# Optimization experiments

Measured on AMD Instinct MI355X. Metric: run time of the kernel, lower is better.

The kernel has to match this reference:

```python
import jax, jax.numpy as jnp
import numpy as np

PRECISION_RATIO = 0.1
ROUTE_THRESH = 0.05

def ternary_quantize(W):
    # TWN-style: delta = 0.7*mean|W|, alpha = mean of kept magnitudes
    delta = 0.7 * jnp.mean(jnp.abs(W))
    mask = (jnp.abs(W) > delta).astype(W.dtype)
    alpha = jnp.sum(jnp.abs(W) * mask) / jnp.maximum(jnp.sum(mask), 1.0)
    return alpha * jnp.sign(W) * mask

def rpb_weight(W, precision_ratio=PRECISION_RATIO):
    # Ternary base + full-precision residual kept for top `precision_ratio` of entries
    Wq = ternary_quantize(W)
    res = W - Wq
    k = max(1, int(precision_ratio * W.size))
    kth = jax.lax.top_k(jnp.abs(res).reshape(-1), k)[0][-1]
    keep = (jnp.abs(res) >= kth).astype(W.dtype)
    return Wq + res * keep

def selective_route(x, threshold=ROUTE_THRESH):
    return x * (jnp.abs(x) >= threshold).astype(x.dtype)

def _lin(x, W, b):
    return x @ W.T + b

def setup_inputs() -> dict:
    key = jax.random.key(0)
    ks = jax.random.split(key, 24)
    B = 8192
    dims = {"vision": 2048, "text": 1024, "audio": 512}
    D = 1024
    T = D * 3  # total_dim = 3072
    s = 0.02
    inp = {
        "x_vision": jax.random.normal(ks[0], (B, dims["vision"]), jnp.float32),
        "x_text": jax.random.normal(ks[1], (B, dims["text"]), jnp.float32),
        "x_audio": jax.random.normal(ks[2], (B, dims["audio"]), jnp.float32),
        "Wv": jax.random.normal(ks[3], (D, dims["vision"]), jnp.float32) * s,
        "bv": jnp.zeros((D,), jnp.float32),
        "Wt": jax.random.normal(ks[4], (D, dims["text"]), jnp.float32) * s,
        "bt": jnp.zeros((D,), jnp.float32),
        "Wa": jax.random.normal(ks[5], (D, dims["audio"]), jnp.float32) * s,
        "ba": jnp.zeros((D,), jnp.float32),
        "Wq1": jax.random.normal(ks[6], (D, T), jnp.float32) * s,
        "bq1": jnp.zeros((D,), jnp.float32),
        "Wq2": jax.random.normal(ks[7], (D, D), jnp.float32) * s,
        "bq2": jnp.zeros((D,), jnp.float32),
        "Wf1": jax.random.normal(ks[8], (D, T), jnp.float32) * s,
        "bf1": jnp.zeros((D,), jnp.float32),
        "Wf2": jax.random.normal(ks[9], (D, D), jnp.float32) * s,
        "bf2": jnp.zeros((D,), jnp.float32),
        "mix_ratio": jnp.asarray(0.75, jnp.float32),
    }
    return inp

def reference(x_vision, x_text, x_audio, Wv, bv, Wt, bt, Wa, ba,
              Wq1, bq1, Wq2, bq2, Wf1, bf1, Wf2, bf2, mix_ratio):
    # per-modality projections then concat in modality order
    pv = _lin(x_vision, Wv, bv)
    pt = _lin(x_text, Wt, bt)
    pa = _lin(x_audio, Wa, ba)
    concat = jnp.concatenate([pv, pt, pa], axis=1)  # [B, 3*D]
    routed = selective_route(concat)
    # quantized (RPB) branch
    h = jax.nn.relu(_lin(routed, rpb_weight(Wq1), bq1))
    out_quant = _lin(h, rpb_weight(Wq2), bq2)
    # full-precision branch
    g = jax.nn.relu(_lin(concat, Wf1, bf1))
    out_full = _lin(g, Wf2, bf2)
    mix = jax.nn.sigmoid(mix_ratio)
    return mix * out_quant + (1.0 - mix) * out_full
```

## Files before the change

### kernel.cpp

```cpp
#include <hip/hip_runtime.h>


typedef _Float16 f16x8 __attribute__((ext_vector_type(8)));
typedef float f32x4 __attribute__((ext_vector_type(4)));

__device__ __forceinline__ unsigned short f16b(float v) {
  union { _Float16 h; unsigned short u; } cv; cv.h = (_Float16)v; return cv.u;
}

__device__ __forceinline__ void load_lds16(const void* g, void* l) {
  __builtin_amdgcn_global_load_lds(
      (const __attribute__((address_space(1))) void*)g,
      (__attribute__((address_space(3))) void*)l, 16, 0, 0);
}

__device__ __forceinline__ float sigmoidf_dev(float x) {
  return 1.0f / (1.0f + expf(-x));
}

#define NB_W1 768
#define NB_TOT 1024

__device__ __forceinline__ float reduce_region_f(const float* part, int lo, int hi,
                                                 float* sbuf) {
  float a = 0.f;
  for (int i = lo + threadIdx.x; i < hi; i += 256) a += part[i];
  sbuf[threadIdx.x] = a; __syncthreads();
  for (int o = 128; o > 0; o >>= 1) {
    if ((int)threadIdx.x < o) sbuf[threadIdx.x] += sbuf[threadIdx.x + o];
    __syncthreads();
  }
  float r = sbuf[0];
  __syncthreads();
  return r;
}

__device__ __forceinline__ float alpha_region(const float* pb, const unsigned* pc,
                                              int lo, int hi, float* sf, unsigned* sc) {
  float a = 0.f; unsigned c = 0;
  for (int i = lo + threadIdx.x; i < hi; i += 256) { a += pb[i]; c += pc[i]; }
  sf[threadIdx.x] = a; sc[threadIdx.x] = c; __syncthreads();
  for (int o = 128; o > 0; o >>= 1) {
    if ((int)threadIdx.x < o) { sf[threadIdx.x] += sf[threadIdx.x + o]; sc[threadIdx.x] += sc[threadIdx.x + o]; }
    __syncthreads();
  }
  float s = sf[0]; float cnt = (float)sc[0];
  __syncthreads();
  if (cnt < 1.f) cnt = 1.f;
  return s / cnt;
}

__device__ __forceinline__ unsigned radix_prefix(const unsigned* __restrict__ hists,
                                                 int w, int nr, unsigned k,
                                                 unsigned* sscan, unsigned* res2) {
  int t = threadIdx.x;
  unsigned prefix = 0, krem = k;
  for (int rr = 0; rr < nr; ++rr) {
    sscan[t] = hists[(rr * 2 + w) * 256 + (255 - t)];
    __syncthreads();
#pragma unroll
    for (int o = 1; o < 256; o <<= 1) {
      unsigned add = (t >= o) ? sscan[t - o] : 0u;
      __syncthreads();
      sscan[t] += add;
      __syncthreads();
    }
    if (sscan[t] >= krem && (t == 0 || sscan[t - 1] < krem)) {
      res2[0] = (unsigned)(255 - t);
      res2[1] = (t == 0) ? 0u : sscan[t - 1];
    }
    __syncthreads();
    prefix |= res2[0] << (24 - 8 * rr);
    krem -= res2[1];
    __syncthreads();
  }
  return prefix;
}

struct Pre1Args {
  const float* src[7];
  unsigned short* dst[7];
  long cum4[8];
  const float* W1; long n41;
  const float* W2; long n42;
  float* part;
  unsigned* hists;
};

__global__ void pre1(Pre1Args a) {
  if (blockIdx.x < 2048) {
    long total = a.cum4[7];
    for (long i = (long)blockIdx.x * 256 + threadIdx.x; i < total;
         i += (long)2048 * 256) {
      int s = 0;
#pragma unroll
      for (int j = 1; j < 7; ++j) s += (i >= a.cum4[j]) ? 1 : 0;
      long off = i - a.cum4[s];
      float4 v = ((const float4*)a.src[s])[off];
      ushort4 o;
      o.x = f16b(v.x); o.y = f16b(v.y); o.z = f16b(v.z); o.w = f16b(v.w);
      ((ushort4*)a.dst[s])[off] = o;
    }
  } else {
    __shared__ float s[256];
    int bid2 = (int)blockIdx.x - 2048;
    if (bid2 < 8) a.hists[bid2 * 256 + threadIdx.x] = 0;
    int w = bid2 < NB_W1 ? 0 : 1;
    const float4* W4 = (const float4*)(w ? a.W2 : a.W1);
    long n4 = w ? a.n42 : a.n41;
    int nb = w ? (NB_TOT - NB_W1) : NB_W1;
    int bid = w ? bid2 - NB_W1 : bid2;
    float acc = 0.f;
    for (long i = (long)bid * 256 + threadIdx.x; i < n4;
         i += (long)nb * 256) {
      float4 v = W4[i];
      acc += fabsf(v.x) + fabsf(v.y) + fabsf(v.z) + fabsf(v.w);
    }
    s[threadIdx.x] = acc; __syncthreads();
    for (int o = 128; o > 0; o >>= 1) {
      if ((int)threadIdx.x < o) s[threadIdx.x] += s[threadIdx.x + o];
      __syncthreads();
    }
    if (threadIdx.x == 0) a.part[bid2] = s[0];
  }
}

__global__ void hist_r(const float* __restrict__ W1, long S1v,
                       const float* __restrict__ W2, long S2v,
                       const float* __restrict__ part,
                       const float* __restrict__ pb, const unsigned* __restrict__ pc,
                       unsigned* __restrict__ hists, int round,
                       unsigned k1, unsigned k2) {
  __shared__ float sf[256]; __shared__ unsigned sc[256];
  __shared__ unsigned h[256]; __shared__ unsigned sscan[256];
  __shared__ unsigned res2[2];
  int t = threadIdx.x;
  int w = blockIdx.x < NB_W1 ? 0 : 1;
  const float* W = w ? W2 : W1;
  long S = w ? S2v : S1v;
  int nb = w ? (NB_TOT - NB_W1) : NB_W1;
  int bid = w ? (int)blockIdx.x - NB_W1 : (int)blockIdx.x;
  int lo = w ? NB_W1 : 0, hi = w ? NB_TOT : NB_W1;
  float tot = reduce_region_f(part, lo, hi, sf);
  float delta = 0.7f * (tot / (float)S);
  float alpha = alpha_region(pb, pc, lo, hi, sf, sc);
  unsigned prefix = radix_prefix(hists, w, round, w ? k2 : k1, sscan, res2);
  h[t] = 0;
  __syncthreads();
  int shift = 24 - 8 * round;
  int hs = shift + 8;
  for (long i = (long)bid * 256 + t; i < S; i += (long)nb * 256) {
    float x = W[i];
    float aw = fabsf(x);
    float wq = (aw > delta) ? copysignf(alpha, x) : 0.0f;
    unsigned ub = __float_as_uint(fabsf(x - wq));
    bool ok = (hs >= 32) || ((ub >> hs) == (prefix >> hs));
    if (ok) atomicAdd(&h[(ub >> shift) & 255u], 1u);
  }
  __syncthreads();
  if (h[t]) atomicAdd(&hists[(round * 2 + w) * 256 + t], h[t]);
}

struct FinArgs {
  const float* Wq1; const float* Wq2; const float* Wf2;
  const float* bq2; const float* bf2; const float* mixp;
  const float* part; const float* pb; const unsigned* pc;
  const unsigned* hists;
  unsigned k1, k2;
  unsigned short* wq1_h;
  unsigned short* w2_h;
  float* b2;
};

__global__ void finalize_weights(FinArgs a) {
  __shared__ float sf[256]; __shared__ unsigned sc[256];
  __shared__ unsigned sscan[256]; __shared__ unsigned res2[2];
  const long S1 = 3145728, S2 = 1048576, D = 1024;
  float tot1 = reduce_region_f(a.part, 0, NB_W1, sf);
  float d1 = 0.7f * (tot1 / (float)S1);
  float tot2 = reduce_region_f(a.part, NB_W1, NB_TOT, sf);
  float d2 = 0.7f * (tot2 / (float)S2);
  float a1 = alpha_region(a.pb, a.pc, 0, NB_W1, sf, sc);
  float a2 = alpha_region(a.pb, a.pc, NB_W1, NB_TOT, sf, sc);
  unsigned kth1 = radix_prefix(a.hists, 0, 4, a.k1, sscan, res2);
  unsigned kth2 = radix_prefix(a.hists, 1, 4, a.k2, sscan, res2);
  float mix = sigmoidf_dev(a.mixp[0]);
  long total = S1 + 2 * S2 + D;
  for (long i = (long)blockIdx.x * blockDim.x + threadIdx.x; i < total;
       i += (long)gridDim.x * blockDim.x) {
    if (i < S1) {
      float x = a.Wq1[i];
      float wq = (fabsf(x) > d1) ? copysignf(a1, x) : 0.0f;
      float res = x - wq;
      float v = wq + ((__float_as_uint(fabsf(res)) >= kth1) ? res : 0.0f);
      a.wq1_h[i] = f16b(v);
    } else if (i < S1 + S2) {
      long j = i - S1; int r = (int)(j >> 10), c = (int)(j & 1023);
      float x = a.Wq2[j];
      float wq = (fabsf(x) > d2) ? copysignf(a2, x) : 0.0f;
      float res = x - wq;
      float v = wq + ((__float_as_uint(fabsf(res)) >= kth2) ? res : 0.0f);
      a.w2_h[(long)r * 2048 + c] = f16b(mix * v);
    } else if (i < S1 + 2 * S2) {
      long j = i - S1 - S2; int r = (int)(j >> 10), c = (int)(j & 1023);
      a.w2_h[(long)r * 2048 + 1024 + c] = f16b((1.0f - mix) * a.Wf2[j]);
    } else {
      long j = i - S1 - 2 * S2;
      a.b2[j] = mix * a.bq2[j] + (1.0f - mix) * a.bf2[j];
    }
  }
}

struct GemmArgs {
  const unsigned short* A0; const unsigned short* A1; const unsigned short* A2;
  const unsigned short* B0; const unsigned short* B1; const unsigned short* B2;
  const float* c0; const float* c1; const float* c2;
  int K0, K1, K2;
  int nrows;
  int ldc;
  int cpsl;
  int nwg;
  unsigned short* o0; unsigned short* o1; float* oF;
  const float* pkW1; long pkS1;
  const float* pkW2; long pkS2;
  const float* pkPart; float* pkPb; unsigned* pkPc;
};

template <int EPI, int BN, bool PK>
__global__ __launch_bounds__(512) void gemm9(GemmArgs g) {
  constexpr int AL = 128 * 32 * 2;
  constexpr int BL = BN * 32 * 2;
  constexpr int BISS = BL / 8192;
  constexpr int NR = BN / 4 / 16;
  __shared__ __align__(16) char sm[2 * AL + 2 * BL];
  const int tid = threadIdx.x;

  if constexpr (PK) {
    if ((int)blockIdx.x >= g.nwg) {
      float* sf = (float*)sm;
      unsigned* sc = (unsigned*)(sm + 2048);
      int bid2 = (int)blockIdx.x - g.nwg;
      int w = bid2 < NB_W1 ? 0 : 1;
      const float* W = w ? g.pkW2 : g.pkW1;
      long S = w ? g.pkS2 : g.pkS1;
      int nb = w ? (NB_TOT - NB_W1) : NB_W1;
      int bid = w ? bid2 - NB_W1 : bid2;
      if (tid < 256) {
        float a = 0.f;
        for (int i = (w ? NB_W1 : 0) + tid; i < (w ? NB_TOT : NB_W1); i += 256)
          a += g.pkPart[i];
        sf[tid] = a;
      }
      __syncthreads();
      for (int o = 128; o > 0; o >>= 1) {
        if (tid < o) sf[tid] += sf[tid + o];
        __syncthreads();
      }
      float delta = 0.7f * (sf[0] / (float)S);
      __syncthreads();
      float a = 0.f; unsigned c = 0;
      for (long i = (long)bid * 512 + tid; i < S; i += (long)nb * 512) {
        float aw = fabsf(W[i]);
        if (aw > delta) { a += aw; ++c; }
      }
      sf[tid] = a; sc[tid] = c; __syncthreads();
      for (int o = 256; o > 0; o >>= 1) {
        if (tid < o) { sf[tid] += sf[tid + o]; sc[tid] += sc[tid + o]; }
        __syncthreads();
      }
      if (tid == 0) { g.pkPb[bid2] = sf[0]; g.pkPc[bid2] = sc[0]; }
      return;
    }
  }

  const int wid = tid >> 6;
  const int lane = tid & 63;
  const int wm = wid >> 2, wn = wid & 3;

  const int nwg = g.nwg;
  const int id = (blockIdx.x & 7) * (nwg >> 3) + (blockIdx.x >> 3);
  const int ncols = nwg / g.nrows;
  const int c = id % ncols, r = id / ncols;
  const int sel = c >> g.cpsl, lc = c & ((1 << g.cpsl) - 1);

  const unsigned short* A = sel == 0 ? g.A0 : (sel == 1 ? g.A1 : g.A2);
  const unsigned short* Bw = sel == 0 ? g.B0 : (sel == 1 ? g.B1 : g.B2);
  const float* bias = sel == 0 ? g.c0 : (sel == 1 ? g.c1 : g.c2);
  const int K = sel == 0 ? g.K0 : (sel == 1 ? g.K1 : g.K2);
  const long brow = (long)r * 128;
  const int bRowB = lc * BN;

  f32x4 acc[4][NR];
#pragma unroll
  for (int i = 0; i < 4; ++i)
#pragma unroll
    for (int j = 0; j < NR; ++j)
#pragma unroll
      for (int e = 0; e < 4; ++e) acc[i][j][e] = 0.f;

  const int oA = tid * 16;
  const unsigned short* aSrc = A + (brow + (oA >> 6)) * (long)K + ((oA & 63) >> 1);
  const unsigned short* bSrc[BISS];
#pragma unroll
  for (int j = 0; j < BISS; ++j) {
    int o = j * 8192 + tid * 16;
    bSrc[j] = Bw + (long)(bRowB + (o >> 6)) * K + ((o & 63) >> 1);
  }

  auto STAGE = [&](int buf, int k0) {
    load_lds16(aSrc + k0, sm + (size_t)buf * AL + wid * 1024);
#pragma unroll
    for (int j = 0; j < BISS; ++j)
      load_lds16(bSrc[j] + k0, sm + 2 * AL + (size_t)buf * BL + j * 8192 + wid * 1024);
  };

  const int kb = (lane >> 4) * 16;
  auto COMPUTE = [&](int buf) {
    const char* lAp = sm + (size_t)buf * AL;
    const char* lBp = sm + 2 * AL + (size_t)buf * BL;
    f16x8 a[4], b[NR];
#pragma unroll
    for (int m = 0; m < 4; ++m)
      a[m] = *(const f16x8*)(lAp + (wm * 64 + m * 16 + (lane & 15)) * 64 + kb);
#pragma unroll
    for (int n = 0; n < NR; ++n)
      b[n] = *(const f16x8*)(lBp + (wn * (BN / 4) + n * 16 + (lane & 15)) * 64 + kb);
#pragma unroll
    for (int m = 0; m < 4; ++m)
#pragma unroll
      for (int n = 0; n < NR; ++n)
        acc[m][n] = __builtin_amdgcn_mfma_f32_16x16x32_f16(a[m], b[n], acc[m][n], 0, 0, 0);
  };

  const int NT = K >> 5;
  STAGE(0, 0);
  __syncthreads();
  int cur = 0;
  for (int t = 0; t < NT - 1; ++t) {
    STAGE(cur ^ 1, (t + 1) << 5);
    COMPUTE(cur);
    __syncthreads();
    cur ^= 1;
  }
  COMPUTE(cur);

  const int cb = c * BN + wn * (BN / 4);
  const int rb = r * 128 + wm * 64;
  const int bcol0 = bRowB + wn * (BN / 4);
#pragma unroll
  for (int i = 0; i < 4; ++i) {
    int r0 = rb + i * 16 + ((lane >> 4) << 2);
#pragma unroll
    for (int j = 0; j < NR; ++j) {
      int ccol = cb + j * 16 + (lane & 15);
      float bb = bias[bcol0 + j * 16 + (lane & 15)];
#pragma unroll
      for (int e = 0; e < 4; ++e) {
        float v = acc[i][j][e] + bb;
        long idx = (long)(r0 + e) * g.ldc + ccol;
        if constexpr (EPI == 0) {
          g.o0[idx] = f16b(v);
          g.o1[idx] = f16b(fabsf(v) >= 0.05f ? v : 0.0f);
        } else if constexpr (EPI == 1) {
          g.o0[idx] = f16b(fmaxf(v, 0.0f));
        } else {
          g.oF[idx] = v;
        }
      }
    }
  }
}

extern "C" void kernel_launch(void* const* d_in, const int* in_sizes, int n_in,
                              void* d_out, int out_size, void* d_ws, size_t ws_size,
                              hipStream_t stream) {
  const float* xv = (const float*)d_in[0];
  const float* xt = (const float*)d_in[1];
  const float* xa = (const float*)d_in[2];
  const float* Wv = (const float*)d_in[3];
  const float* bv = (const float*)d_in[4];
  const float* Wt = (const float*)d_in[5];
  const float* bt = (const float*)d_in[6];
  const float* Wa = (const float*)d_in[7];
  const float* ba = (const float*)d_in[8];
  const float* Wq1 = (const float*)d_in[9];
  const float* bq1 = (const float*)d_in[10];
  const float* Wq2 = (const float*)d_in[11];
  const float* bq2 = (const float*)d_in[12];
  const float* Wf1 = (const float*)d_in[13];
  const float* bf1 = (const float*)d_in[14];
  const float* Wf2 = (const float*)d_in[15];
  const float* bf2 = (const float*)d_in[16];
  const float* mixp = (const float*)d_in[17];

  const int B = 8192, D = 1024, T = 3072;
  const int Kv = 2048, Kt = 1024, Ka = 512;
  const long S1 = (long)D * T, S2 = (long)D * D;

  char* w = (char*)d_ws;
  auto alloc = [&](size_t bytes) -> char* {
    char* p = w; w += (bytes + 255) & ~(size_t)255; return p;
  };
  unsigned short* xv_h = (unsigned short*)alloc((size_t)B * Kv * 2);
  unsigned short* xt_h = (unsigned short*)alloc((size_t)B * Kt * 2);
  unsigned short* xa_h = (unsigned short*)alloc((size_t)B * Ka * 2);
  unsigned short* wv_h = (unsigned short*)alloc((size_t)D * Kv * 2);
  unsigned short* wt_h = (unsigned short*)alloc((size_t)D * Kt * 2);
  unsigned short* wa_h = (unsigned short*)alloc((size_t)D * Ka * 2);
  unsigned short* wq1_h = (unsigned short*)alloc((size_t)D * T * 2);
  unsigned short* wf1_h = (unsigned short*)alloc((size_t)D * T * 2);
  unsigned short* w2_h = (unsigned short*)alloc((size_t)D * 2048 * 2);
  unsigned short* concat_h = (unsigned short*)alloc((size_t)B * T * 2);
  unsigned short* routed_h = (unsigned short*)alloc((size_t)B * T * 2);
  unsigned short* a2_h = (unsigned short*)alloc((size_t)B * 2048 * 2);
  float* b2 = (float*)alloc(D * 4);
  float* part = (float*)alloc(1024 * 4);
  float* pb = (float*)alloc(1024 * 4);
  unsigned* pc = (unsigned*)alloc(1024 * 4);
  unsigned* hists = (unsigned*)alloc(4 * 2 * 256 * 4);

  const unsigned k1 = (unsigned)(S1 / 10), k2 = (unsigned)(S2 / 10);

  Pre1Args pa;
  pa.src[0] = xv;  pa.dst[0] = xv_h;
  pa.src[1] = xt;  pa.dst[1] = xt_h;
  pa.src[2] = xa;  pa.dst[2] = xa_h;
  pa.src[3] = Wv;  pa.dst[3] = wv_h;
  pa.src[4] = Wt;  pa.dst[4] = wt_h;
  pa.src[5] = Wa;  pa.dst[5] = wa_h;
  pa.src[6] = Wf1; pa.dst[6] = wf1_h;
  long n4s[7] = {(long)B * Kv / 4, (long)B * Kt / 4, (long)B * Ka / 4,
                 (long)D * Kv / 4, (long)D * Kt / 4, (long)D * Ka / 4, S1 / 4};
  pa.cum4[0] = 0;
  for (int i = 0; i < 7; ++i) pa.cum4[i + 1] = pa.cum4[i] + n4s[i];
  pa.W1 = Wq1; pa.n41 = S1 / 4;
  pa.W2 = Wq2; pa.n42 = S2 / 4;
  pa.part = part; pa.hists = hists;
  pre1<<<3072, 256, 0, stream>>>(pa);

  GemmArgs gp;
  gp.A0 = xv_h; gp.A1 = xt_h; gp.A2 = xa_h;
  gp.B0 = wv_h; gp.B1 = wt_h; gp.B2 = wa_h;
  gp.c0 = bv; gp.c1 = bt; gp.c2 = ba;
  gp.K0 = Kv; gp.K1 = Kt; gp.K2 = Ka;
  gp.nrows = B / 128; gp.ldc = T; gp.cpsl = 2; gp.nwg = 12 * (B / 128);
  gp.o0 = concat_h; gp.o1 = routed_h; gp.oF = nullptr;
  gp.pkW1 = Wq1; gp.pkS1 = S1;
  gp.pkW2 = Wq2; gp.pkS2 = S2;
  gp.pkPart = part; gp.pkPb = pb; gp.pkPc = pc;
  gemm9<0, 256, true><<<gp.nwg + NB_TOT, 512, 0, stream>>>(gp);

  for (int rr = 0; rr < 4; ++rr)
    hist_r<<<NB_TOT, 256, 0, stream>>>(Wq1, S1, Wq2, S2, part, pb, pc,
                                       hists, rr, k1, k2);

  FinArgs fw;
  fw.Wq1 = Wq1; fw.Wq2 = Wq2; fw.Wf2 = Wf2;
  fw.bq2 = bq2; fw.bf2 = bf2; fw.mixp = mixp;
  fw.part = part; fw.pb = pb; fw.pc = pc; fw.hists = hists;
  fw.k1 = k1; fw.k2 = k2;
  fw.wq1_h = wq1_h; fw.w2_h = w2_h; fw.b2 = b2;
  finalize_weights<<<1024, 256, 0, stream>>>(fw);

  GemmArgs gh;
  gh.A0 = routed_h; gh.A1 = concat_h; gh.A2 = routed_h;
  gh.B0 = wq1_h; gh.B1 = wf1_h; gh.B2 = wq1_h;
  gh.c0 = bq1; gh.c1 = bf1; gh.c2 = bq1;
  gh.K0 = T; gh.K1 = T; gh.K2 = T;
  gh.nrows = B / 128; gh.ldc = 2048; gh.cpsl = 2; gh.nwg = 8 * (B / 128);
  gh.o0 = a2_h; gh.o1 = nullptr; gh.oF = nullptr;
  gemm9<1, 256, false><<<gh.nwg, 512, 0, stream>>>(gh);

  GemmArgs gf;
  gf.A0 = a2_h; gf.A1 = a2_h; gf.A2 = a2_h;
  gf.B0 = w2_h; gf.B1 = w2_h; gf.B2 = w2_h;
  gf.c0 = b2; gf.c1 = b2; gf.c2 = b2;
  gf.K0 = 2048; gf.K1 = 2048; gf.K2 = 2048;
  gf.nrows = B / 128; gf.ldc = D; gf.cpsl = 3; gf.nwg = 8 * (B / 128);
  gf.o0 = nullptr; gf.o1 = nullptr; gf.oF = (float*)d_out;
  gemm9<2, 128, false><<<gf.nwg, 512, 0, stream>>>(gf);
}
```

Baseline: 393.5 us.

## Use 256x256-tile GEMM kernel for first hidden-layer matmul

Adds a new gemm8f kernel that computes 256x256 output tiles with 8 waves, each wave owning a 128x64 sub-tile, and splits every K step into two MFMA halves. Global-to-LDS loads of A and B for later steps are issued between those halves, with explicit waitcnt and barriers. The first hidden-layer GEMM is switched from the 128-row gemm9 to this kernel, which halves the workgroup count and raises operand reuse per LDS load. In exchange it needs more accumulator registers (128 floats per lane) and uses fewer workgroups on the GPU, so occupancy and tail balance could suffer.

```diff
diff --git a/kernel.cpp b/kernel.cpp
--- a/kernel.cpp
+++ b/kernel.cpp
@@ -226,6 +226,138 @@
   const float* pkPart; float* pkPb; unsigned* pkPc;
 };
 
+template <int EPI>
+__global__ __launch_bounds__(512) void gemm8f(GemmArgs g) {
+  constexpr int QB = 8192;
+  constexpr int BUF = 4 * QB;
+  __shared__ __align__(16) char sm[2 * BUF];
+  const int tid = threadIdx.x;
+  const int wid = tid >> 6, lane = tid & 63;
+  const int wm = wid >> 2, wn = wid & 3;
+  const int l15 = lane & 15, l4 = lane >> 4;
+
+  const int nwg = g.nwg;
+  const int id = (blockIdx.x & 7) * (nwg >> 3) + (blockIdx.x >> 3);
+  const int ncols = nwg / g.nrows;
+  const int c = id % ncols, r = id / ncols;
+  const int sel = c >> g.cpsl, lc = c & ((1 << g.cpsl) - 1);
+
+  const unsigned short* A = sel == 0 ? g.A0 : (sel == 1 ? g.A1 : g.A2);
+  const unsigned short* Bw = sel == 0 ? g.B0 : (sel == 1 ? g.B1 : g.B2);
+  const float* bias = sel == 0 ? g.c0 : (sel == 1 ? g.c1 : g.c2);
+  const int K = sel == 0 ? g.K0 : (sel == 1 ? g.K1 : g.K2);
+  const long brow = (long)r * 256;
+  const int bRowB = lc * 256;
+
+  f32x4 acc[8][4];
+#pragma unroll
+  for (int i = 0; i < 8; ++i)
+#pragma unroll
+    for (int j = 0; j < 4; ++j)
+#pragma unroll
+      for (int e = 0; e < 4; ++e) acc[i][j][e] = 0.f;
+
+  const int qr = tid & 127, kc = tid >> 7;
+  const unsigned short* srcA[2];
+  const unsigned short* srcB[2];
+#pragma unroll
+  for (int q = 0; q < 2; ++q) {
+    srcA[q] = A + (brow + q * 128 + qr) * (long)K + kc * 8;
+    srcB[q] = Bw + (long)(bRowB + q * 128 + qr) * K + kc * 8;
+  }
+
+  auto STAGE_A = [&](int buf, int k0) {
+#pragma unroll
+    for (int q = 0; q < 2; ++q)
+      load_lds16(srcA[q] + k0, sm + (size_t)buf * BUF + q * QB + wid * 1024);
+  };
+  auto STAGE_B = [&](int buf, int k0) {
+#pragma unroll
+    for (int q = 0; q < 2; ++q)
+      load_lds16(srcB[q] + k0, sm + (size_t)buf * BUF + 2 * QB + q * QB + wid * 1024);
+  };
+
+  const int aQ = wm * QB;
+  const int bQ = 2 * QB + (wn >> 1) * QB;
+  const int bR0 = (wn & 1) * 64;
+  auto RD = [&](int buf, int qoff, int rowl) -> f16x8 {
+    return *(const f16x8*)(sm + (size_t)buf * BUF + qoff + l4 * 2048 + rowl * 16);
+  };
+
+  const int NT = K >> 5;
+  STAGE_A(0, 0);
+  STAGE_B(0, 0);
+  STAGE_A(1, 32);
+  asm volatile("s_waitcnt vmcnt(2)" ::: "memory");
+  __builtin_amdgcn_s_barrier();
+  __builtin_amdgcn_sched_barrier(0);
+
+  for (int t = 0; t < NT; ++t) {
+    const int buf = t & 1, obuf = buf ^ 1;
+    f16x8 a[8], b0, b1, b2, b3;
+    b0 = RD(buf, bQ, bR0 + l15);
+    b1 = RD(buf, bQ, bR0 + 16 + l15);
+#pragma unroll
+    for (int m = 0; m < 8; ++m) a[m] = RD(buf, aQ, m * 16 + l15);
+    if (t + 1 < NT) STAGE_B(obuf, (t + 1) << 5);
+    __builtin_amdgcn_s_barrier();
+    asm volatile("s_waitcnt lgkmcnt(0)" ::: "memory");
+    __builtin_amdgcn_sched_barrier(0);
+    __builtin_amdgcn_s_setprio(1);
+#pragma unroll
+    for (int m = 0; m < 8; ++m) {
+      acc[m][0] = __builtin_amdgcn_mfma_f32_16x16x32_f16(a[m], b0, acc[m][0], 0, 0, 0);
+      acc[m][1] = __builtin_amdgcn_mfma_f32_16x16x32_f16(a[m], b1, acc[m][1], 0, 0, 0);
+    }
+    __builtin_amdgcn_s_setprio(0);
+    __builtin_amdgcn_s_barrier();
+    __builtin_amdgcn_sched_barrier(0);
+    b2 = RD(buf, bQ, bR0 + 32 + l15);
+    b3 = RD(buf, bQ, bR0 + 48 + l15);
+    if (t + 2 < NT) STAGE_A(buf, (t + 2) << 5);
+    __builtin_amdgcn_s_barrier();
+    asm volatile("s_waitcnt lgkmcnt(0)" ::: "memory");
+    __builtin_amdgcn_sched_barrier(0);
+    __builtin_amdgcn_s_setprio(1);
+#pragma unroll
+    for (int m = 0; m < 8; ++m) {
+      acc[m][2] = __builtin_amdgcn_mfma_f32_16x16x32_f16(a[m], b2, acc[m][2], 0, 0, 0);
+      acc[m][3] = __builtin_amdgcn_mfma_f32_16x16x32_f16(a[m], b3, acc[m][3], 0, 0, 0);
+    }
+    __builtin_amdgcn_s_setprio(0);
+    if (t + 1 < NT) {
+      if (t + 2 < NT) asm volatile("s_waitcnt vmcnt(2)" ::: "memory");
+      else            asm volatile("s_waitcnt vmcnt(0)" ::: "memory");
+      __builtin_amdgcn_s_barrier();
+      __builtin_amdgcn_sched_barrier(0);
+    }
+  }
+
+  const int cb = c * 256 + wn * 64;
+  const int rb = r * 256 + wm * 128;
+  const int bcol0 = bRowB + wn * 64;
+#pragma unroll
+  for (int m = 0; m < 8; ++m) {
+    int r0 = rb + m * 16 + (l4 << 2);
+#pragma unroll
+    for (int n = 0; n < 4; ++n) {
+      int ccol = cb + n * 16 + l15;
+      float bb = bias[bcol0 + n * 16 + l15];
+#pragma unroll
+      for (int e = 0; e < 4; ++e) {
+        float v = acc[m][n][e] + bb;
+        long idx = (long)(r0 + e) * g.ldc + ccol;
+        if constexpr (EPI == 0) {
+          g.o0[idx] = f16b(v);
+          g.o1[idx] = f16b(fabsf(v) >= 0.05f ? v : 0.0f);
+        } else {
+          g.o0[idx] = f16b(fmaxf(v, 0.0f));
+        }
+      }
+    }
+  }
+}
+
 template <int EPI, int BN, bool PK>
 __global__ __launch_bounds__(512) void gemm9(GemmArgs g) {
   constexpr int AL = 128 * 32 * 2;
@@ -467,9 +599,9 @@
   gh.B0 = wq1_h; gh.B1 = wf1_h; gh.B2 = wq1_h;
   gh.c0 = bq1; gh.c1 = bf1; gh.c2 = bq1;
   gh.K0 = T; gh.K1 = T; gh.K2 = T;
-  gh.nrows = B / 128; gh.ldc = 2048; gh.cpsl = 2; gh.nwg = 8 * (B / 128);
+  gh.nrows = B / 256; gh.ldc = 2048; gh.cpsl = 2; gh.nwg = 8 * (B / 256);
   gh.o0 = a2_h; gh.o1 = nullptr; gh.oF = nullptr;
-  gemm9<1, 256, false><<<gh.nwg, 512, 0, stream>>>(gh);
+  gemm8f<1><<<gh.nwg, 512, 0, stream>>>(gh);
 
   GemmArgs gf;
   gf.A0 = a2_h; gf.A1 = a2_h; gf.A2 = a2_h;
```

New measurement: 414.4 us. 1.05x slower.
